# Kernel optimization log

Measured on AMD Instinct MI355X. Metric: run time of the kernel, lower is better.

## Reference

```python
import jax, jax.numpy as jnp
import numpy as np

N, E, R = 50000, 300000, 4
F_IN, H, G, T = 11, 256, 2048, 19
BN_EPS = 1e-5


def _init_lin(key, fan_in, fan_out, extra=()):
    k1, k2 = jax.random.split(key)
    s = 1.0 / np.sqrt(fan_in)
    W = jax.random.uniform(k1, extra + (fan_in, fan_out), jnp.float32, -s, s)
    b = jax.random.uniform(k2, extra + (fan_out,), jnp.float32, -s, s)
    return W, b


def setup_inputs() -> dict:
    key = jax.random.key(0)
    ks = jax.random.split(key, 32)
    inp = {
        "x": jax.random.normal(ks[0], (N, F_IN), jnp.float32),
        "edge_index": jax.random.randint(ks[1], (2, E), 0, N, jnp.int64),
        "edge_type": jax.random.randint(ks[2], (E,), 0, R, jnp.int64),
        "batch": jnp.sort(jax.random.randint(ks[3], (N,), 0, G, jnp.int64)),
    }
    ki = 4
    for li, fin in ((1, F_IN), (2, H), (3, H)):
        sw, sb = _init_lin(ks[ki], fin, H); ki += 1
        w1, b1 = _init_lin(ks[ki], fin, H, (R,)); ki += 1
        w2, b2 = _init_lin(ks[ki], H, H, (R,)); ki += 1
        inp[f"l{li}_sw"], inp[f"l{li}_sb"] = sw, sb
        inp[f"l{li}_w1"], inp[f"l{li}_b1"] = w1, b1
        inp[f"l{li}_g"] = jnp.ones((R, H), jnp.float32)
        inp[f"l{li}_bt"] = jnp.zeros((R, H), jnp.float32)
        inp[f"l{li}_w2"], inp[f"l{li}_b2"] = w2, b2
    inp["lin_w"], inp["lin_b"] = _init_lin(ks[ki], H, T)
    return inp


def _rgin_layer(x, src, dst, rel_mask, sw, sb, w1, b1, g, bt, w2, b2):
    # self-loop linear
    out = x @ sw + sb
    msg = x[src]  # [E, d] gather of source features
    for i in range(R):
        # per-relation masked scatter-add aggregation at target nodes
        agg = jax.ops.segment_sum(msg * rel_mask[:, i:i + 1], dst, num_segments=N)
        h = x + agg  # GIN with eps=0: (1+eps)*x + sum_neighbors
        h = h @ w1[i] + b1[i]
        # BatchNorm1d (training-mode batch stats, biased var)
        mu = jnp.mean(h, axis=0)
        var = jnp.var(h, axis=0)
        h = (h - mu) * jax.lax.rsqrt(var + BN_EPS) * g[i] + bt[i]
        h = jax.nn.relu(h)
        out = out + h @ w2[i] + b2[i]
    return out


def reference(x, edge_index, edge_type, batch,
              l1_sw, l1_sb, l1_w1, l1_b1, l1_g, l1_bt, l1_w2, l1_b2,
              l2_sw, l2_sb, l2_w1, l2_b1, l2_g, l2_bt, l2_w2, l2_b2,
              l3_sw, l3_sb, l3_w1, l3_b1, l3_g, l3_bt, l3_w2, l3_b2,
              lin_w, lin_b):
    src, dst = edge_index[0], edge_index[1]
    rel_mask = jax.nn.one_hot(edge_type, R, dtype=x.dtype)  # [E, R]
    h = jax.nn.relu(_rgin_layer(x, src, dst, rel_mask, l1_sw, l1_sb, l1_w1, l1_b1, l1_g, l1_bt, l1_w2, l1_b2))
    h = jax.nn.relu(_rgin_layer(h, src, dst, rel_mask, l2_sw, l2_sb, l2_w1, l2_b1, l2_g, l2_bt, l2_w2, l2_b2))
    h = jax.nn.relu(_rgin_layer(h, src, dst, rel_mask, l3_sw, l3_sb, l3_w1, l3_b1, l3_g, l3_bt, l3_w2, l3_b2))
    # global mean pool over graphs
    pooled = jax.ops.segment_sum(h, batch, num_segments=G)
    counts = jax.ops.segment_sum(jnp.ones((N,), h.dtype), batch, num_segments=G)
    pooled = pooled / jnp.maximum(counts, 1.0)[:, None]
    return pooled @ lin_w + lin_b
```

## Files before the change

### kernel.cpp

```cpp
#include <hip/hip_runtime.h>

static const int kN = 50000;
static const int kE = 300000;
static const int kG = 2048;
static const int kT = 19;
static const int kSeg = kN * 4;
static const int kScanB = (kSeg + 256) / 256;

typedef __bf16 bf16;
typedef __bf16 bf16x8 __attribute__((ext_vector_type(8)));
typedef __bf16 bf16x4 __attribute__((ext_vector_type(4)));
typedef float  f32x4  __attribute__((ext_vector_type(4)));

__global__ __launch_bounds__(512) void k_rgin1(
    const bf16* __restrict__ Pb, const int* __restrict__ srcidx,
    const int* __restrict__ row_ptr, const bf16* __restrict__ w1t,
    bf16* __restrict__ h1, float* __restrict__ stats)
{
    __shared__ bf16 As[64][264];
    const int t = threadIdx.x;
    const int r = blockIdx.y;
    const int m0 = blockIdx.x * 64;
    const int wave = t >> 6, lane = t & 63;
    const int l15 = lane & 15, lq = lane >> 4, koff = lq * 8;
    const int wn = wave * 32;

    const bf16* Bt = w1t + (long)r * 65536;
    const bf16* Bp[2];
#pragma unroll
    for (int j = 0; j < 2; ++j)
        Bp[j] = Bt + (long)(wn + j * 16 + l15) * 256 + koff;
    bf16x8 b0[2], b1[2];
#pragma unroll
    for (int j = 0; j < 2; ++j) b0[j] = *(const bf16x8*)(Bp[j]);

    {
        const int rbase = m0 + wave * 8;
        int i0s[8], i1s[8];
#pragma unroll
        for (int rr = 0; rr < 8; ++rr) {
            int dc = rbase + rr; if (dc >= kN) dc = kN - 1;
            int seg = dc * 4 + r;
            i0s[rr] = row_ptr[seg];
            i1s[rr] = row_ptr[seg + 1];
        }
#pragma unroll
        for (int rr = 0; rr < 8; ++rr) {
            int dc = rbase + rr; if (dc >= kN) dc = kN - 1;
            bf16x4 sv = ((const bf16x4*)(Pb + (long)dc * 256))[lane];
            f32x4 a = {(float)sv[0], (float)sv[1], (float)sv[2], (float)sv[3]};
            int i = i0s[rr], i1 = i1s[rr];
            for (; i + 1 < i1; i += 2) {
                int s0 = srcidx[i], s1 = srcidx[i + 1];
                bf16x4 v0 = ((const bf16x4*)(Pb + (long)s0 * 256))[lane];
                bf16x4 v1 = ((const bf16x4*)(Pb + (long)s1 * 256))[lane];
                a[0] += (float)v0[0] + (float)v1[0];
                a[1] += (float)v0[1] + (float)v1[1];
                a[2] += (float)v0[2] + (float)v1[2];
                a[3] += (float)v0[3] + (float)v1[3];
            }
            if (i < i1) {
                bf16x4 v0 = ((const bf16x4*)(Pb + (long)srcidx[i] * 256))[lane];
                a[0] += (float)v0[0]; a[1] += (float)v0[1];
                a[2] += (float)v0[2]; a[3] += (float)v0[3];
            }
            bf16x4 o = {(bf16)a[0], (bf16)a[1], (bf16)a[2], (bf16)a[3]};
            *(bf16x4*)&As[wave * 8 + rr][lane * 4] = o;
        }
    }
    __syncthreads();

    const bf16* Ar[4];
#pragma unroll
    for (int i = 0; i < 4; ++i) Ar[i] = &As[i * 16 + l15][koff];

    f32x4 acc[4][2];
#pragma unroll
    for (int i = 0; i < 4; ++i)
#pragma unroll
        for (int j = 0; j < 2; ++j) acc[i][j] = (f32x4){0.f, 0.f, 0.f, 0.f};

#pragma unroll
    for (int kt = 0; kt < 256; kt += 32) {
        int kn = kt + 32; if (kn >= 256) kn = 0;
#pragma unroll
        for (int j = 0; j < 2; ++j) b1[j] = *(const bf16x8*)(Bp[j] + kn);
        bf16x8 a[4];
#pragma unroll
        for (int i = 0; i < 4; ++i) a[i] = *(const bf16x8*)(Ar[i] + kt);
#pragma unroll
        for (int i = 0; i < 4; ++i)
#pragma unroll
            for (int j = 0; j < 2; ++j)
                acc[i][j] = __builtin_amdgcn_mfma_f32_16x16x32_bf16(a[i], b0[j], acc[i][j], 0, 0, 0);
#pragma unroll
        for (int j = 0; j < 2; ++j) b0[j] = b1[j];
    }

    const int cB = r * 256;
    float sv[2] = {0, 0}, qv[2] = {0, 0};
#pragma unroll
    for (int i = 0; i < 4; ++i) {
        int rowb = m0 + i * 16 + lq * 4;
#pragma unroll
        for (int rr = 0; rr < 4; ++rr) {
            int gm = rowb + rr;
            if (gm < kN) {
#pragma unroll
                for (int j = 0; j < 2; ++j) {
                    int gn = wn + j * 16 + l15;
                    bf16 bv = (bf16)acc[i][j][rr];
                    h1[(long)gm * 1024 + cB + gn] = bv;
                    float f = (float)bv;
                    sv[j] += f; qv[j] += f * f;
                }
            }
        }
    }
#pragma unroll
    for (int j = 0; j < 2; ++j) {
        float s = sv[j], q = qv[j];
        s += __shfl_xor(s, 16); s += __shfl_xor(s, 32);
        q += __shfl_xor(q, 16); q += __shfl_xor(q, 32);
        if (lq == 0) {
            int gn = cB + wn + j * 16 + l15;
            atomicAdd(&stats[gn], s);
            atomicAdd(&stats[1024 + gn], q);
        }
    }
}

__global__ __launch_bounds__(512) void k_l1gemm(
    const bf16* __restrict__ a1b, const bf16* __restrict__ w1tL1,
    bf16* __restrict__ h1, float* __restrict__ stats)
{
    const int t = threadIdx.x;
    const int r = blockIdx.y;
    const int m0 = blockIdx.x * 128;
    const int wave = t >> 6, lane = t & 63;
    const int l15 = lane & 15, lq = lane >> 4, koff = lq * 8;
    const int wm = (wave & 1) * 64, wn = (wave >> 1) * 64;

    bf16x8 a[4], b[4];
#pragma unroll
    for (int i = 0; i < 4; ++i) {
        int gm = m0 + wm + i * 16 + l15;
        if (gm >= kN) gm = kN - 1;
        a[i] = *(const bf16x8*)(a1b + ((long)r * kN + gm) * 32 + koff);
    }
#pragma unroll
    for (int j = 0; j < 4; ++j)
        b[j] = *(const bf16x8*)(w1tL1 + (long)r * 8192 + (long)(wn + j * 16 + l15) * 32 + koff);

    f32x4 acc[4][4];
#pragma unroll
    for (int i = 0; i < 4; ++i)
#pragma unroll
        for (int j = 0; j < 4; ++j)
            acc[i][j] = __builtin_amdgcn_mfma_f32_16x16x32_bf16(a[i], b[j],
                        (f32x4){0.f, 0.f, 0.f, 0.f}, 0, 0, 0);

    const int cB = r * 256;
    float sv[4] = {0,0,0,0}, qv[4] = {0,0,0,0};
#pragma unroll
    for (int i = 0; i < 4; ++i) {
        int rowb = m0 + wm + i * 16 + lq * 4;
#pragma unroll
        for (int rr = 0; rr < 4; ++rr) {
            int gm = rowb + rr;
            if (gm < kN) {
#pragma unroll
                for (int j = 0; j < 4; ++j) {
                    int gn = wn + j * 16 + l15;
                    bf16 bv = (bf16)acc[i][j][rr];
                    h1[(long)gm * 1024 + cB + gn] = bv;
                    float f = (float)bv;
                    sv[j] += f; qv[j] += f * f;
                }
            }
        }
    }
#pragma unroll
    for (int j = 0; j < 4; ++j) {
        float s = sv[j], q = qv[j];
        s += __shfl_xor(s, 16); s += __shfl_xor(s, 32);
        q += __shfl_xor(q, 16); q += __shfl_xor(q, 32);
        if (lq == 0) {
            int gn = cB + wn + j * 16 + l15;
            atomicAdd(&stats[gn], s);
            atomicAdd(&stats[1024 + gn], q);
        }
    }
}

template<int CHUNKS, int C1, bool PoolOut>
__global__ __launch_bounds__(256) void k_gemm2(
    const bf16* __restrict__ A1, int lda1,
    const bf16* __restrict__ A2,
    const bf16* __restrict__ Bt,
    bf16* __restrict__ Cout,
    int M, const float* __restrict__ bias,
    const float* __restrict__ scl, const float* __restrict__ shf,
    const int* __restrict__ batch, float* __restrict__ pooled)
{
    constexpr int K  = CHUNKS * 128;
    constexpr int KS = CHUNKS * 4;
    __shared__ bf16 As[2][64][136];
    const int t = threadIdx.x;
    const int wave = t >> 6, lane = t & 63;
    const int l15 = lane & 15, lq = lane >> 4, koff = lq * 8;
    const int wn = wave * 64;
    const int m0 = blockIdx.x * 64;

    const int srow = t >> 4;
    const int kg   = (t & 15) * 8;

    const bf16* Bp[4];
#pragma unroll
    for (int j = 0; j < 4; ++j)
        Bp[j] = Bt + (long)(wave * 4 + j) * KS * 512 + lane * 8;

    f32x4 acc[4][4];
#pragma unroll
    for (int i = 0; i < 4; ++i)
#pragma unroll
        for (int j = 0; j < 4; ++j) acc[i][j] = (f32x4){0.f, 0.f, 0.f, 0.f};

    auto ld_raw = [&](int c, bf16x8* rv, float4* sf) {
#pragma unroll
        for (int i = 0; i < 4; ++i) {
            int gm = m0 + srow + i * 16; if (gm >= M) gm = M - 1;
            if (c < C1) rv[i] = *(const bf16x8*)(A1 + (long)gm * lda1 + c * 128 + kg);
            else        rv[i] = *(const bf16x8*)(A2 + (long)gm * 1024 + (c - C1) * 128 + kg);
        }
        if (c >= C1) {
            int k2 = (c - C1) * 128 + kg;
            sf[0] = *(const float4*)(scl + k2);
            sf[1] = *(const float4*)(scl + k2 + 4);
            sf[2] = *(const float4*)(shf + k2);
            sf[3] = *(const float4*)(shf + k2 + 4);
        }
    };
    auto st_lds = [&](int c, const bf16x8* rv, const float4* sf, int sel) {
        float sa[8], ta[8];
        if (c >= C1) {
            sa[0]=sf[0].x; sa[1]=sf[0].y; sa[2]=sf[0].z; sa[3]=sf[0].w;
            sa[4]=sf[1].x; sa[5]=sf[1].y; sa[6]=sf[1].z; sa[7]=sf[1].w;
            ta[0]=sf[2].x; ta[1]=sf[2].y; ta[2]=sf[2].z; ta[3]=sf[2].w;
            ta[4]=sf[3].x; ta[5]=sf[3].y; ta[6]=sf[3].z; ta[7]=sf[3].w;
        }
#pragma unroll
        for (int i = 0; i < 4; ++i) {
            bf16x8 v = rv[i];
            if (c >= C1) {
                bf16x8 o;
#pragma unroll
                for (int u = 0; u < 8; ++u)
                    o[u] = (bf16)fmaxf(0.f, fmaf((float)v[u], sa[u], ta[u]));
                v = o;
            }
            *(bf16x8*)&As[sel][srow + i * 16][kg] = v;
        }
    };

    bf16x8 rv[4]; float4 sf[4];
    ld_raw(0, rv, sf);
    bf16x8 breg[2][4];
#pragma unroll
    for (int j = 0; j < 4; ++j) breg[0][j] = *(const bf16x8*)(Bp[j]);
#pragma unroll
    for (int j = 0; j < 4; ++j) breg[1][j] = *(const bf16x8*)(Bp[j] + 512);
    st_lds(0, rv, sf, 0);
    __syncthreads();

    for (int c = 0; c < CHUNKS; ++c) {
        const int sel = c & 1;
        if (c + 1 < CHUNKS) ld_raw(c + 1, rv, sf);
#pragma unroll
        for (int ks = 0; ks < 4; ++ks) {
            bf16x8 a[4], bu[4];
#pragma unroll
            for (int i = 0; i < 4; ++i)
                a[i] = *(const bf16x8*)&As[sel][i * 16 + l15][ks * 32 + koff];
#pragma unroll
            for (int j = 0; j < 4; ++j) bu[j] = breg[ks & 1][j];
            int knext = c * 4 + ks + 2; if (knext >= KS) knext = 0;
#pragma unroll
            for (int j = 0; j < 4; ++j)
                breg[ks & 1][j] = *(const bf16x8*)(Bp[j] + (long)knext * 512);
#pragma unroll
            for (int i = 0; i < 4; ++i)
#pragma unroll
                for (int j = 0; j < 4; ++j)
                    acc[i][j] = __builtin_amdgcn_mfma_f32_16x16x32_bf16(a[i], bu[j], acc[i][j], 0, 0, 0);
        }
        if (c + 1 < CHUNKS) {
            st_lds(c + 1, rv, sf, sel ^ 1);
            __syncthreads();
        }
    }

#pragma unroll
    for (int i = 0; i < 4; ++i) {
        int rowb = m0 + i * 16 + lq * 4;
#pragma unroll
        for (int rr = 0; rr < 4; ++rr) {
            int gm = rowb + rr;
            if (gm < M) {
                int g = PoolOut ? batch[gm] : 0;
#pragma unroll
                for (int j = 0; j < 4; ++j) {
                    int gn = wn + j * 16 + l15;
                    float v = fmaxf(acc[i][j][rr] + bias[gn], 0.f);
                    if (PoolOut) atomicAdd(&pooled[(long)g * 256 + gn], v);
                    else         Cout[(long)gm * 256 + gn] = (bf16)v;
                }
            }
        }
    }
}

__global__ void k_hist(const int* __restrict__ ei, const int* __restrict__ et,
                       int* __restrict__ hist)
{
    int e = blockIdx.x * 256 + threadIdx.x;
    if (e >= kE) return;
    atomicAdd(&hist[ei[kE + e] * 4 + et[e]], 1);
}

__global__ void k_scan1(const int* __restrict__ hist, int* __restrict__ bsum)
{
    __shared__ int sd[256];
    int i = blockIdx.x * 256 + threadIdx.x;
    sd[threadIdx.x] = (i < kSeg) ? hist[i] : 0;
    __syncthreads();
    for (int o = 128; o > 0; o >>= 1) {
        if (threadIdx.x < o) sd[threadIdx.x] += sd[threadIdx.x + o];
        __syncthreads();
    }
    if (threadIdx.x == 0) bsum[blockIdx.x] = sd[0];
}

__global__ __launch_bounds__(1024) void k_scan2(const int* __restrict__ bsum,
                                                int* __restrict__ boff)
{
    __shared__ int sd[1024];
    int t = threadIdx.x;
    sd[t] = (t < kScanB) ? bsum[t] : 0;
    __syncthreads();
    for (int o = 1; o < 1024; o <<= 1) {
        int v = (t >= o) ? sd[t - o] : 0;
        __syncthreads();
        sd[t] += v;
        __syncthreads();
    }
    if (t < kScanB) boff[t] = (t == 0) ? 0 : sd[t - 1];
}

__global__ void k_scan3(const int* __restrict__ hist, const int* __restrict__ boff,
                        int* __restrict__ row_ptr, int* __restrict__ cursor)
{
    __shared__ int sd[256];
    int i = blockIdx.x * 256 + threadIdx.x;
    int v = (i < kSeg) ? hist[i] : 0;
    sd[threadIdx.x] = v;
    __syncthreads();
    for (int o = 1; o < 256; o <<= 1) {
        int u = (threadIdx.x >= o) ? sd[threadIdx.x - o] : 0;
        __syncthreads();
        sd[threadIdx.x] += u;
        __syncthreads();
    }
    if (i <= kSeg) {
        int excl = boff[blockIdx.x] + sd[threadIdx.x] - v;
        row_ptr[i] = excl;
        if (i < kSeg) cursor[i] = excl;
    }
}

__global__ void k_fill(const int* __restrict__ ei, const int* __restrict__ et,
                       int* __restrict__ cursor, int* __restrict__ srcidx)
{
    int e = blockIdx.x * 256 + threadIdx.x;
    if (e >= kE) return;
    int key = ei[kE + e] * 4 + et[e];
    int pos = atomicAdd(&cursor[key], 1);
    srcidx[pos] = ei[e];
}

__global__ void k_agg11(const float* __restrict__ x, const int* __restrict__ srcidx,
                        const int* __restrict__ row_ptr, bf16* __restrict__ a1b)
{
    long gid = (long)blockIdx.x * 256 + threadIdx.x;
    if (gid >= (long)kSeg * 32) return;
    int ch  = (int)(gid & 31);
    int seg = (int)(gid >> 5);
    int d = seg >> 2, r = seg & 3;
    float acc = 0.f;
    if (ch < 11) {
        acc = x[(long)d * 11 + ch];
        int i0 = row_ptr[seg], i1 = row_ptr[seg + 1];
        for (int i = i0; i < i1; ++i) acc += x[(long)srcidx[i] * 11 + ch];
    }
    a1b[((long)r * kN + d) * 32 + ch] = (bf16)acc;
}

__global__ void k_xpad(const float* __restrict__ x, bf16* __restrict__ xb1)
{
    long gid = (long)blockIdx.x * 256 + threadIdx.x;
    if (gid >= (long)kN * 128) return;
    int c = (int)(gid & 127); long d = gid >> 7;
    xb1[gid] = (c < 11) ? (bf16)x[d * 11 + c] : (bf16)0.f;
}

__global__ void k_wt_s(const float* __restrict__ in, bf16* __restrict__ out,
                       int K, int N, int ldout, int coff)
{
    int i = blockIdx.x * 256 + threadIdx.x;
    if (i >= K * N) return;
    int n = i / K, k = i - n * K;
    out[(long)n * ldout + coff + k] = (bf16)in[(long)k * N + n];
}

__global__ void k_wt_f(const float* __restrict__ in, bf16* __restrict__ out,
                       int Kin, int k0, int KS)
{
    int i = blockIdx.x * 256 + threadIdx.x;
    if (i >= Kin * 256) return;
    int n = i & 255, krel = i >> 8;
    int k = k0 + krel;
    int blk = ((n >> 6) * 4 + ((n >> 4) & 3)) * KS + (k >> 5);
    int idx = blk * 512 + ((k >> 3) & 3) * 128 + (n & 15) * 8 + (k & 7);
    out[idx] = (bf16)in[(long)krel * 256 + n];
}

__global__ void k_wtL1(const float* __restrict__ w1, bf16* __restrict__ out)
{
    int i = blockIdx.x * 256 + threadIdx.x;
    if (i >= 4 * 256 * 32) return;
    int r = i >> 13, rem = i & 8191, n = rem >> 5, k = rem & 31;
    out[i] = (k < 11) ? (bf16)w1[(long)r * 11 * 256 + (long)k * 256 + n] : (bf16)0.f;
}

__global__ void k_bn_params(const float* __restrict__ stats,
                            const float* __restrict__ g, const float* __restrict__ bt,
                            float* __restrict__ scl, float* __restrict__ shf)
{
    int c = blockIdx.x * 256 + threadIdx.x;
    const float invN = 1.0f / (float)kN;
    float mu  = stats[c] * invN;
    float var = stats[1024 + c] * invN - mu * mu;
    float sc  = g[c] * rsqrtf(var + 1e-5f);
    scl[c] = sc;
    shf[c] = bt[c] - mu * sc;
}

__global__ void k_bias_total(const float* sb0, const float* b20,
                             const float* sb1, const float* b21,
                             const float* sb2, const float* b22,
                             float* __restrict__ btt)
{
    int l = blockIdx.x, j = threadIdx.x;
    const float* sb = (l == 0) ? sb0 : (l == 1) ? sb1 : sb2;
    const float* b2 = (l == 0) ? b20 : (l == 1) ? b21 : b22;
    float v = sb[j];
#pragma unroll
    for (int r = 0; r < 4; ++r) v += b2[r * 256 + j];
    btt[l * 256 + j] = v;
}

__global__ void k_counts(const int* __restrict__ batch, float* __restrict__ counts)
{
    int v = blockIdx.x * 256 + threadIdx.x;
    if (v < kN) atomicAdd(&counts[batch[v]], 1.0f);
}

__global__ __launch_bounds__(64) void k_head(const float* __restrict__ pooled,
                                             const float* __restrict__ counts,
                                             const float* __restrict__ lw,
                                             const float* __restrict__ lb,
                                             float* __restrict__ out)
{
    int g = blockIdx.x;
    int l = threadIdx.x;
    float inv = 1.0f / fmaxf(counts[g], 1.0f);
    float acc[kT];
#pragma unroll
    for (int t = 0; t < kT; ++t) acc[t] = 0.f;
    for (int k = l; k < 256; k += 64) {
        float p = pooled[((long)g << 8) + k] * inv;
#pragma unroll
        for (int t = 0; t < kT; ++t) acc[t] = fmaf(p, lw[k * kT + t], acc[t]);
    }
#pragma unroll
    for (int off = 32; off > 0; off >>= 1)
#pragma unroll
        for (int t = 0; t < kT; ++t) acc[t] += __shfl_down(acc[t], off);
    if (l == 0) {
#pragma unroll
        for (int t = 0; t < kT; ++t) out[(long)g * kT + t] = acc[t] + lb[t];
    }
}

extern "C" void kernel_launch(void* const* d_in, const int* in_sizes, int n_in,
                              void* d_out, int out_size, void* d_ws, size_t ws_size,
                              hipStream_t stream)
{
    const float* x     = (const float*)d_in[0];
    const int*   ei    = (const int*)d_in[1];
    const int*   et    = (const int*)d_in[2];
    const int*   batch = (const int*)d_in[3];

    const float *sw[3], *sb[3], *w1[3], *gmm[3], *btm[3], *w2[3], *b2[3];
    for (int l = 0; l < 3; ++l) {
        int b = 4 + l * 8;
        sw[l]  = (const float*)d_in[b + 0];
        sb[l]  = (const float*)d_in[b + 1];
        w1[l]  = (const float*)d_in[b + 2];
        gmm[l] = (const float*)d_in[b + 4];
        btm[l] = (const float*)d_in[b + 5];
        w2[l]  = (const float*)d_in[b + 6];
        b2[l]  = (const float*)d_in[b + 7];
    }
    const float* lin_w = (const float*)d_in[28];
    const float* lin_b = (const float*)d_in[29];
    float* out = (float*)d_out;
    (void)in_sizes; (void)n_in; (void)out_size;

    char* wsb = (char*)d_ws;
    size_t off = 0;
    auto alloc = [&](size_t bytes) { void* p = wsb + off; off = (off + bytes + 255) & ~(size_t)255; return p; };
    bf16*  Pb0    = (bf16*) alloc((size_t)kN * 256 * 2);
    bf16*  Pb1    = (bf16*) alloc((size_t)kN * 256 * 2);
    bf16*  h1     = (bf16*) alloc((size_t)kN * 1024 * 2);
    bf16*  a1b    = (bf16*) alloc((size_t)4 * kN * 32 * 2);
    bf16*  xb1    = (bf16*) alloc((size_t)kN * 128 * 2);
    bf16*  w1t    = (bf16*) alloc((size_t)2 * 4 * 65536 * 2);
    bf16*  w1tL1  = (bf16*) alloc((size_t)4 * 256 * 32 * 2);
    bf16*  Bc0    = (bf16*) alloc((size_t)256 * 1152 * 2);
    bf16*  Bc1    = (bf16*) alloc((size_t)256 * 1280 * 2);
    bf16*  Bc2    = (bf16*) alloc((size_t)256 * 1280 * 2);
    int*   hist   = (int*)  alloc((size_t)(kSeg + 1) * 4);
    int*   row_ptr= (int*)  alloc((size_t)(kSeg + 1) * 4);
    int*   cursor = (int*)  alloc((size_t)kSeg * 4);
    int*   srcidx = (int*)  alloc((size_t)kE * 4);
    int*   bsum   = (int*)  alloc((size_t)kScanB * 4);
    int*   boff   = (int*)  alloc((size_t)kScanB * 4);
    float* stats  = (float*)alloc(2048 * 4);
    float* scl    = (float*)alloc(1024 * 4);
    float* shf    = (float*)alloc(1024 * 4);
    float* btt    = (float*)alloc(3 * 256 * 4);
    float* pooled = (float*)alloc((size_t)kG * 256 * 4);
    float* counts = (float*)alloc(kG * 4);
    if (ws_size < off) return;

    const dim3 gL1((kN + 127) / 128, 4);
    const dim3 gR((kN + 63) / 64, 4);
    const dim3 g2((kN + 63) / 64);

    hipMemsetAsync(hist, 0, (size_t)(kSeg + 1) * 4, stream);
    k_hist<<<(kE + 255) / 256, 256, 0, stream>>>(ei, et, hist);
    k_scan1<<<kScanB, 256, 0, stream>>>(hist, bsum);
    k_scan2<<<1, 1024, 0, stream>>>(bsum, boff);
    k_scan3<<<kScanB, 256, 0, stream>>>(hist, boff, row_ptr, cursor);
    k_fill<<<(kE + 255) / 256, 256, 0, stream>>>(ei, et, cursor, srcidx);

    k_bias_total<<<3, 256, 0, stream>>>(sb[0], b2[0], sb[1], b2[1], sb[2], b2[2], btt);
    k_xpad<<<(int)(((long)kN * 128 + 255) / 256), 256, 0, stream>>>(x, xb1);
    k_wtL1<<<(4 * 256 * 32 + 255) / 256, 256, 0, stream>>>(w1[0], w1tL1);
    for (int l = 1; l < 3; ++l)
        for (int r = 0; r < 4; ++r)
            k_wt_s<<<256, 256, 0, stream>>>(w1[l] + (long)r * 65536,
                                            w1t + (long)(l - 1) * 4 * 65536 + (long)r * 65536,
                                            256, 256, 256, 0);
    hipMemsetAsync(Bc0, 0, (size_t)256 * 1152 * 2, stream);
    k_wt_f<<<(11 * 256 + 255) / 256, 256, 0, stream>>>(sw[0], Bc0, 11, 0, 36);
    k_wt_f<<<1024, 256, 0, stream>>>(w2[0], Bc0, 1024, 128, 36);
    k_wt_f<<<256, 256, 0, stream>>>(sw[1], Bc1, 256, 0, 40);
    k_wt_f<<<1024, 256, 0, stream>>>(w2[1], Bc1, 1024, 256, 40);
    k_wt_f<<<256, 256, 0, stream>>>(sw[2], Bc2, 256, 0, 40);
    k_wt_f<<<1024, 256, 0, stream>>>(w2[2], Bc2, 1024, 256, 40);

    k_counts<<<(kN + 255) / 256, 256, 0, stream>>>(batch, counts);
    hipMemsetAsync(pooled, 0, (size_t)kG * 256 * 4, stream);

    k_agg11<<<(int)(((long)kSeg * 32 + 255) / 256), 256, 0, stream>>>(x, srcidx, row_ptr, a1b);
    hipMemsetAsync(stats, 0, 2048 * 4, stream);
    k_l1gemm<<<gL1, 512, 0, stream>>>(a1b, w1tL1, h1, stats);
    k_bn_params<<<4, 256, 0, stream>>>(stats, gmm[0], btm[0], scl, shf);
    k_gemm2<9, 1, false><<<g2, 256, 0, stream>>>(xb1, 128, h1, Bc0,
                                                 Pb0, kN, btt + 0, scl, shf, nullptr, nullptr);

    hipMemsetAsync(stats, 0, 2048 * 4, stream);
    k_rgin1<<<gR, 512, 0, stream>>>(Pb0, srcidx, row_ptr, w1t, h1, stats);
    k_bn_params<<<4, 256, 0, stream>>>(stats, gmm[1], btm[1], scl, shf);
    k_gemm2<10, 2, false><<<g2, 256, 0, stream>>>(Pb0, 256, h1, Bc1,
                                                  Pb1, kN, btt + 256, scl, shf, nullptr, nullptr);

    hipMemsetAsync(stats, 0, 2048 * 4, stream);
    k_rgin1<<<gR, 512, 0, stream>>>(Pb1, srcidx, row_ptr, w1t + (size_t)4 * 65536, h1, stats);
    k_bn_params<<<4, 256, 0, stream>>>(stats, gmm[2], btm[2], scl, shf);
    k_gemm2<10, 2, true><<<g2, 256, 0, stream>>>(Pb1, 256, h1, Bc2,
                                                 nullptr, kN, btt + 512, scl, shf, batch, pooled);

    k_head<<<kG, 64, 0, stream>>>(pooled, counts, lin_w, lin_b, out);
}
```

Measured before the change: 913.2 us.

## Hand-schedule gemm2 main loop with explicit waitcnts, setprio, and LDS-cached BN params

Rewrites the k_gemm2 K-loop as unrolled phases. Each phase reads A from LDS, waits only on specific vmcnt levels for the prefetched B registers, and issues the MFMAs under raised priority, with sched_barriers fixing the order. The BN scale/shift vectors are staged once into LDS instead of reloaded from global per chunk, and the last chunk is peeled so it issues no wasted prefetch. The aim is tighter overlap of global loads with MFMA work, at the cost of fragile hand-counted vmcnt values and extra LDS use.

Measured after the change: 888.1 us, median of 3. -2.8%, faster.

```diff
diff --git a/kernel.cpp b/kernel.cpp
--- a/kernel.cpp
+++ b/kernel.cpp
@@ -193,6 +193,24 @@
     }
 }
 
+#define KS_PHASE(SEL, KSI, BREG, VM) do {                                     \
+    bf16x8 a_[4];                                                             \
+    _Pragma("unroll")                                                         \
+    for (int i_ = 0; i_ < 4; ++i_)                                            \
+        a_[i_] = *(const bf16x8*)&As[SEL][i_ * 16 + l15][(KSI) * 32 + koff];  \
+    asm volatile("s_waitcnt vmcnt(" #VM ")" ::: "memory");                    \
+    __builtin_amdgcn_sched_barrier(0);                                        \
+    __builtin_amdgcn_s_setprio(1);                                            \
+    _Pragma("unroll")                                                         \
+    for (int i_ = 0; i_ < 4; ++i_)                                            \
+        _Pragma("unroll")                                                     \
+        for (int j_ = 0; j_ < 4; ++j_)                                        \
+            acc[i_][j_] = __builtin_amdgcn_mfma_f32_16x16x32_bf16(            \
+                a_[i_], BREG[j_], acc[i_][j_], 0, 0, 0);                      \
+    __builtin_amdgcn_s_setprio(0);                                            \
+    __builtin_amdgcn_sched_barrier(0);                                        \
+} while (0)
+
 template<int CHUNKS, int C1, bool PoolOut>
 __global__ __launch_bounds__(256) void k_gemm2(
     const bf16* __restrict__ A1, int lda1,
@@ -203,9 +221,10 @@
     const float* __restrict__ scl, const float* __restrict__ shf,
     const int* __restrict__ batch, float* __restrict__ pooled)
 {
-    constexpr int K  = CHUNKS * 128;
     constexpr int KS = CHUNKS * 4;
     __shared__ bf16 As[2][64][136];
+    __shared__ float sclL[1024];
+    __shared__ float shfL[1024];
     const int t = threadIdx.x;
     const int wave = t >> 6, lane = t & 63;
     const int l15 = lane & 15, lq = lane >> 4, koff = lq * 8;
@@ -226,78 +245,101 @@
 #pragma unroll
         for (int j = 0; j < 4; ++j) acc[i][j] = (f32x4){0.f, 0.f, 0.f, 0.f};
 
-    auto ld_raw = [&](int c, bf16x8* rv, float4* sf) {
+    bf16x8 rv[4];
+    auto ld_A = [&](int c) {
 #pragma unroll
         for (int i = 0; i < 4; ++i) {
             int gm = m0 + srow + i * 16; if (gm >= M) gm = M - 1;
-            if (c < C1) rv[i] = *(const bf16x8*)(A1 + (long)gm * lda1 + c * 128 + kg);
-            else        rv[i] = *(const bf16x8*)(A2 + (long)gm * 1024 + (c - C1) * 128 + kg);
-        }
+            const bf16* p = (c < C1)
+                ? (A1 + (long)gm * lda1 + c * 128 + kg)
+                : (A2 + (long)gm * 1024 + (c - C1) * 128 + kg);
+            rv[i] = *(const bf16x8*)p;
+        }
+    };
+    auto st_lds = [&](int c, int sel) {
         if (c >= C1) {
             int k2 = (c - C1) * 128 + kg;
-            sf[0] = *(const float4*)(scl + k2);
-            sf[1] = *(const float4*)(scl + k2 + 4);
-            sf[2] = *(const float4*)(shf + k2);
-            sf[3] = *(const float4*)(shf + k2 + 4);
-        }
-    };
-    auto st_lds = [&](int c, const bf16x8* rv, const float4* sf, int sel) {
-        float sa[8], ta[8];
-        if (c >= C1) {
-            sa[0]=sf[0].x; sa[1]=sf[0].y; sa[2]=sf[0].z; sa[3]=sf[0].w;
-            sa[4]=sf[1].x; sa[5]=sf[1].y; sa[6]=sf[1].z; sa[7]=sf[1].w;
-            ta[0]=sf[2].x; ta[1]=sf[2].y; ta[2]=sf[2].z; ta[3]=sf[2].w;
-            ta[4]=sf[3].x; ta[5]=sf[3].y; ta[6]=sf[3].z; ta[7]=sf[3].w;
-        }
-#pragma unroll
-        for (int i = 0; i < 4; ++i) {
-            bf16x8 v = rv[i];
-            if (c >= C1) {
-                bf16x8 o;
+            float4 s0 = *(const float4*)&sclL[k2];
+            float4 s1 = *(const float4*)&sclL[k2 + 4];
+            float4 t0 = *(const float4*)&shfL[k2];
+            float4 t1 = *(const float4*)&shfL[k2 + 4];
+            float sa[8] = {s0.x, s0.y, s0.z, s0.w, s1.x, s1.y, s1.z, s1.w};
+            float ta[8] = {t0.x, t0.y, t0.z, t0.w, t1.x, t1.y, t1.z, t1.w};
+#pragma unroll
+            for (int i = 0; i < 4; ++i) {
+                bf16x8 v = rv[i]; bf16x8 o;
 #pragma unroll
                 for (int u = 0; u < 8; ++u)
                     o[u] = (bf16)fmaxf(0.f, fmaf((float)v[u], sa[u], ta[u]));
-                v = o;
+                *(bf16x8*)&As[sel][srow + i * 16][kg] = o;
             }
-            *(bf16x8*)&As[sel][srow + i * 16][kg] = v;
+        } else {
+#pragma unroll
+            for (int i = 0; i < 4; ++i)
+                *(bf16x8*)&As[sel][srow + i * 16][kg] = rv[i];
         }
     };
 
-    bf16x8 rv[4]; float4 sf[4];
-    ld_raw(0, rv, sf);
-    bf16x8 breg[2][4];
-#pragma unroll
-    for (int j = 0; j < 4; ++j) breg[0][j] = *(const bf16x8*)(Bp[j]);
-#pragma unroll
-    for (int j = 0; j < 4; ++j) breg[1][j] = *(const bf16x8*)(Bp[j] + 512);
-    st_lds(0, rv, sf, 0);
-    __syncthreads();
-
-    for (int c = 0; c < CHUNKS; ++c) {
+    bf16x8 breg0[4], breg1[4];
+
+    {
+        const float* src = (t < 128) ? (scl + t * 8) : (shf + (t - 128) * 8);
+        float*       dst = (t < 128) ? (sclL + t * 8) : (shfL + (t - 128) * 8);
+        float4 f0 = *(const float4*)src;
+        float4 f1 = *(const float4*)(src + 4);
+        ld_A(0);
+#pragma unroll
+        for (int j = 0; j < 4; ++j) breg0[j] = *(const bf16x8*)(Bp[j]);
+#pragma unroll
+        for (int j = 0; j < 4; ++j) breg1[j] = *(const bf16x8*)(Bp[j] + 512);
+        asm volatile("s_waitcnt vmcnt(12)" ::: "memory");
+        __builtin_amdgcn_sched_barrier(0);
+        *(float4*)dst = f0; *(float4*)(dst + 4) = f1;
+        asm volatile("s_waitcnt vmcnt(8)" ::: "memory");
+        __builtin_amdgcn_sched_barrier(0);
+        st_lds(0, 0);
+        asm volatile("s_waitcnt lgkmcnt(0)" ::: "memory");
+        __builtin_amdgcn_s_barrier();
+    }
+
+    for (int c = 0; c < CHUNKS - 1; ++c) {
         const int sel = c & 1;
-        if (c + 1 < CHUNKS) ld_raw(c + 1, rv, sf);
-#pragma unroll
-        for (int ks = 0; ks < 4; ++ks) {
-            bf16x8 a[4], bu[4];
-#pragma unroll
-            for (int i = 0; i < 4; ++i)
-                a[i] = *(const bf16x8*)&As[sel][i * 16 + l15][ks * 32 + koff];
-#pragma unroll
-            for (int j = 0; j < 4; ++j) bu[j] = breg[ks & 1][j];
-            int knext = c * 4 + ks + 2; if (knext >= KS) knext = 0;
-#pragma unroll
-            for (int j = 0; j < 4; ++j)
-                breg[ks & 1][j] = *(const bf16x8*)(Bp[j] + (long)knext * 512);
-#pragma unroll
-            for (int i = 0; i < 4; ++i)
-#pragma unroll
-                for (int j = 0; j < 4; ++j)
-                    acc[i][j] = __builtin_amdgcn_mfma_f32_16x16x32_bf16(a[i], bu[j], acc[i][j], 0, 0, 0);
-        }
-        if (c + 1 < CHUNKS) {
-            st_lds(c + 1, rv, sf, sel ^ 1);
-            __syncthreads();
-        }
+        KS_PHASE(sel, 0, breg0, 4);
+#pragma unroll
+        for (int j = 0; j < 4; ++j)
+            breg0[j] = *(const bf16x8*)(Bp[j] + (long)(4 * c + 2) * 512);
+        ld_A(c + 1);
+        KS_PHASE(sel, 1, breg1, 8);
+#pragma unroll
+        for (int j = 0; j < 4; ++j)
+            breg1[j] = *(const bf16x8*)(Bp[j] + (long)(4 * c + 3) * 512);
+        KS_PHASE(sel, 2, breg0, 8);
+#pragma unroll
+        for (int j = 0; j < 4; ++j)
+            breg0[j] = *(const bf16x8*)(Bp[j] + (long)(4 * c + 4) * 512);
+        KS_PHASE(sel, 3, breg1, 4);
+#pragma unroll
+        for (int j = 0; j < 4; ++j)
+            breg1[j] = *(const bf16x8*)(Bp[j] + (long)(4 * c + 5) * 512);
+        asm volatile("s_waitcnt vmcnt(8)" ::: "memory");
+        __builtin_amdgcn_sched_barrier(0);
+        st_lds(c + 1, sel ^ 1);
+        asm volatile("s_waitcnt lgkmcnt(0)" ::: "memory");
+        __builtin_amdgcn_s_barrier();
+    }
+
+    {
+        const int c = CHUNKS - 1, sel = c & 1;
+        KS_PHASE(sel, 0, breg0, 4);
+#pragma unroll
+        for (int j = 0; j < 4; ++j)
+            breg0[j] = *(const bf16x8*)(Bp[j] + (long)(4 * c + 2) * 512);
+        KS_PHASE(sel, 1, breg1, 4);
+#pragma unroll
+        for (int j = 0; j < 4; ++j)
+            breg1[j] = *(const bf16x8*)(Bp[j] + (long)(4 * c + 3) * 512);
+        KS_PHASE(sel, 2, breg0, 4);
+        KS_PHASE(sel, 3, breg1, 0);
     }
 
 #pragma unroll
```

## Halve gemm2 row tile and stage K in two halves with swizzled LDS

Applied to the files above, without the earlier changes.

The second-stage GEMM drops from 64-row to 32-row blocks, doubling the grid. Instead of double-buffered 128-wide K chunks with a barrier per chunk, it loads half of the K range into LDS, syncs, computes, then loads the second half. LDS addressing uses an XOR swizzle to avoid bank conflicts. This cuts barriers and accumulator registers so more blocks can be resident, but each block reuses the B operand over fewer rows and global loads no longer overlap with the MFMA work.

Measured after the change: 1.105 ms. 21.0% more time.

```diff
diff --git a/kernel.cpp b/kernel.cpp
--- a/kernel.cpp
+++ b/kernel.cpp
@@ -203,105 +203,106 @@
     const float* __restrict__ scl, const float* __restrict__ shf,
     const int* __restrict__ batch, float* __restrict__ pooled)
 {
-    constexpr int K  = CHUNKS * 128;
-    constexpr int KS = CHUNKS * 4;
-    __shared__ bf16 As[2][64][136];
+    constexpr int KS   = CHUNKS * 4;
+    constexpr int HC0  = (CHUNKS + 1) / 2;
+    constexpr int ROWB = HC0 * 256;
+    __shared__ bf16 As[32 * HC0 * 128];
+
     const int t = threadIdx.x;
     const int wave = t >> 6, lane = t & 63;
     const int l15 = lane & 15, lq = lane >> 4, koff = lq * 8;
     const int wn = wave * 64;
-    const int m0 = blockIdx.x * 64;
-
+    const int m0 = blockIdx.x * 32;
     const int srow = t >> 4;
     const int kg   = (t & 15) * 8;
 
+    auto lds_off = [&](int row, int colrel) {
+        return row * ROWB + ((colrel * 2) ^ ((row & 7) << 4));
+    };
+
     const bf16* Bp[4];
 #pragma unroll
     for (int j = 0; j < 4; ++j)
         Bp[j] = Bt + (long)(wave * 4 + j) * KS * 512 + lane * 8;
 
-    f32x4 acc[4][4];
-#pragma unroll
-    for (int i = 0; i < 4; ++i)
+    f32x4 acc[2][4];
+#pragma unroll
+    for (int i = 0; i < 2; ++i)
 #pragma unroll
         for (int j = 0; j < 4; ++j) acc[i][j] = (f32x4){0.f, 0.f, 0.f, 0.f};
 
-    auto ld_raw = [&](int c, bf16x8* rv, float4* sf) {
-#pragma unroll
-        for (int i = 0; i < 4; ++i) {
-            int gm = m0 + srow + i * 16; if (gm >= M) gm = M - 1;
-            if (c < C1) rv[i] = *(const bf16x8*)(A1 + (long)gm * lda1 + c * 128 + kg);
-            else        rv[i] = *(const bf16x8*)(A2 + (long)gm * 1024 + (c - C1) * 128 + kg);
-        }
-        if (c >= C1) {
-            int k2 = (c - C1) * 128 + kg;
-            sf[0] = *(const float4*)(scl + k2);
-            sf[1] = *(const float4*)(scl + k2 + 4);
-            sf[2] = *(const float4*)(shf + k2);
-            sf[3] = *(const float4*)(shf + k2 + 4);
-        }
-    };
-    auto st_lds = [&](int c, const bf16x8* rv, const float4* sf, int sel) {
-        float sa[8], ta[8];
-        if (c >= C1) {
-            sa[0]=sf[0].x; sa[1]=sf[0].y; sa[2]=sf[0].z; sa[3]=sf[0].w;
-            sa[4]=sf[1].x; sa[5]=sf[1].y; sa[6]=sf[1].z; sa[7]=sf[1].w;
-            ta[0]=sf[2].x; ta[1]=sf[2].y; ta[2]=sf[2].z; ta[3]=sf[2].w;
-            ta[4]=sf[3].x; ta[5]=sf[3].y; ta[6]=sf[3].z; ta[7]=sf[3].w;
-        }
-#pragma unroll
-        for (int i = 0; i < 4; ++i) {
-            bf16x8 v = rv[i];
-            if (c >= C1) {
-                bf16x8 o;
-#pragma unroll
-                for (int u = 0; u < 8; ++u)
-                    o[u] = (bf16)fmaxf(0.f, fmaf((float)v[u], sa[u], ta[u]));
-                v = o;
+    bf16x8 breg0[4], breg1[4];
+#pragma unroll
+    for (int j = 0; j < 4; ++j) breg0[j] = *(const bf16x8*)(Bp[j]);
+#pragma unroll
+    for (int j = 0; j < 4; ++j) breg1[j] = *(const bf16x8*)(Bp[j] + 512);
+
+#define KSTEP(GKS_, BREG_) do {                                               \
+    const int colrel_ = ((GKS_) - c0 * 4) * 32 + koff;                        \
+    bf16x8 a0_ = *(const bf16x8*)((const char*)As + lds_off(l15, colrel_));   \
+    bf16x8 a1_ = *(const bf16x8*)((const char*)As + lds_off(16 + l15, colrel_)); \
+    bf16x8 bu_[4];                                                            \
+    _Pragma("unroll")                                                         \
+    for (int j_ = 0; j_ < 4; ++j_) bu_[j_] = BREG_[j_];                       \
+    int nk_ = (GKS_) + 2; if (nk_ >= KS) nk_ = 0;                             \
+    _Pragma("unroll")                                                         \
+    for (int j_ = 0; j_ < 4; ++j_)                                            \
+        BREG_[j_] = *(const bf16x8*)(Bp[j_] + (long)nk_ * 512);               \
+    _Pragma("unroll")                                                         \
+    for (int j_ = 0; j_ < 4; ++j_) {                                          \
+        acc[0][j_] = __builtin_amdgcn_mfma_f32_16x16x32_bf16(a0_, bu_[j_], acc[0][j_], 0, 0, 0); \
+        acc[1][j_] = __builtin_amdgcn_mfma_f32_16x16x32_bf16(a1_, bu_[j_], acc[1][j_], 0, 0, 0); \
+    }                                                                         \
+} while (0)
+
+#pragma unroll
+    for (int h = 0; h < 2; ++h) {
+        const int c0 = h ? HC0 : 0;
+        const int cN = h ? CHUNKS : HC0;
+#pragma unroll
+        for (int cc = 0; cc < cN - c0; ++cc) {
+            const int c = c0 + cc;
+            const int col = c * 128 + kg;
+            if (c < C1) {
+#pragma unroll
+                for (int p = 0; p < 2; ++p) {
+                    int gm = m0 + srow + p * 16; if (gm >= M) gm = M - 1;
+                    bf16x8 v = *(const bf16x8*)(A1 + (long)gm * lda1 + col);
+                    *(bf16x8*)((char*)As + lds_off(srow + p * 16, cc * 128 + kg)) = v;
+                }
+            } else {
+                const int k2 = col - C1 * 128;
+                float4 s0 = *(const float4*)(scl + k2);
+                float4 s1 = *(const float4*)(scl + k2 + 4);
+                float4 t0 = *(const float4*)(shf + k2);
+                float4 t1 = *(const float4*)(shf + k2 + 4);
+                float sa[8] = {s0.x,s0.y,s0.z,s0.w,s1.x,s1.y,s1.z,s1.w};
+                float ta[8] = {t0.x,t0.y,t0.z,t0.w,t1.x,t1.y,t1.z,t1.w};
+#pragma unroll
+                for (int p = 0; p < 2; ++p) {
+                    int gm = m0 + srow + p * 16; if (gm >= M) gm = M - 1;
+                    bf16x8 v = *(const bf16x8*)(A2 + (long)gm * 1024 + k2);
+                    bf16x8 o;
+#pragma unroll
+                    for (int u = 0; u < 8; ++u)
+                        o[u] = (bf16)fmaxf(0.f, fmaf((float)v[u], sa[u], ta[u]));
+                    *(bf16x8*)((char*)As + lds_off(srow + p * 16, cc * 128 + kg)) = o;
+                }
             }
-            *(bf16x8*)&As[sel][srow + i * 16][kg] = v;
-        }
-    };
-
-    bf16x8 rv[4]; float4 sf[4];
-    ld_raw(0, rv, sf);
-    bf16x8 breg[2][4];
-#pragma unroll
-    for (int j = 0; j < 4; ++j) breg[0][j] = *(const bf16x8*)(Bp[j]);
-#pragma unroll
-    for (int j = 0; j < 4; ++j) breg[1][j] = *(const bf16x8*)(Bp[j] + 512);
-    st_lds(0, rv, sf, 0);
-    __syncthreads();
-
-    for (int c = 0; c < CHUNKS; ++c) {
-        const int sel = c & 1;
-        if (c + 1 < CHUNKS) ld_raw(c + 1, rv, sf);
-#pragma unroll
-        for (int ks = 0; ks < 4; ++ks) {
-            bf16x8 a[4], bu[4];
-#pragma unroll
-            for (int i = 0; i < 4; ++i)
-                a[i] = *(const bf16x8*)&As[sel][i * 16 + l15][ks * 32 + koff];
-#pragma unroll
-            for (int j = 0; j < 4; ++j) bu[j] = breg[ks & 1][j];
-            int knext = c * 4 + ks + 2; if (knext >= KS) knext = 0;
-#pragma unroll
-            for (int j = 0; j < 4; ++j)
-                breg[ks & 1][j] = *(const bf16x8*)(Bp[j] + (long)knext * 512);
-#pragma unroll
-            for (int i = 0; i < 4; ++i)
-#pragma unroll
-                for (int j = 0; j < 4; ++j)
-                    acc[i][j] = __builtin_amdgcn_mfma_f32_16x16x32_bf16(a[i], bu[j], acc[i][j], 0, 0, 0);
-        }
-        if (c + 1 < CHUNKS) {
-            st_lds(c + 1, rv, sf, sel ^ 1);
-            __syncthreads();
-        }
-    }
-
-#pragma unroll
-    for (int i = 0; i < 4; ++i) {
+        }
+        __syncthreads();
+        const int nks = (cN - c0) * 4;
+#pragma unroll
+        for (int s = 0; s < nks; s += 2) {
+            KSTEP(c0 * 4 + s,     breg0);
+            KSTEP(c0 * 4 + s + 1, breg1);
+        }
+        if (h == 0) __syncthreads();
+    }
+#undef KSTEP
+
+#pragma unroll
+    for (int i = 0; i < 2; ++i) {
         int rowb = m0 + i * 16 + lq * 4;
 #pragma unroll
         for (int rr = 0; rr < 4; ++rr) {
@@ -556,7 +557,7 @@
 
     const dim3 gL1((kN + 127) / 128, 4);
     const dim3 gR((kN + 63) / 64, 4);
-    const dim3 g2((kN + 63) / 64);
+    const dim3 g2((kN + 31) / 32);
 
     hipMemsetAsync(hist, 0, (size_t)(kSeg + 1) * 4, stream);
     k_hist<<<(kE + 255) / 256, 256, 0, stream>>>(ei, et, hist);
```

## Store h1 in MFMA fragment layout, fold BN scale into W2, drop LDS staging

Applied to the files above, without the earlier changes.

The first GEMM outputs and the padded input are now written in a pre-tiled MFMA A-fragment layout, so the second GEMM loads fragments straight from global memory without LDS staging or barriers. The BatchNorm scale is folded into the W2 weights, which are rebuilt after each stats pass, so the activation transform reduces to an add followed by ReLU. The intent is to remove shared-memory traffic, synchronisation and per-element FMA work from the main GEMM. In exchange it adds scattered 2-byte stores in the producers and extra weight-repack launches. The identity bt/sc - mu breaks down if the scale is zero or negative, and the fixed-size fragment buffer relies on the padded panel count.

New measurement: 1.121 ms. +22.8%, slower.

```diff
diff --git a/kernel.cpp b/kernel.cpp
--- a/kernel.cpp
+++ b/kernel.cpp
@@ -12,10 +12,15 @@
 typedef __bf16 bf16x4 __attribute__((ext_vector_type(4)));
 typedef float  f32x4  __attribute__((ext_vector_type(4)));
 
+__device__ __forceinline__ long fragA_idx(int row, int k, int KSR) {
+    return ((long)(row >> 4) * KSR + (k >> 5)) * 512
+         + ((k >> 3) & 3) * 128 + (row & 15) * 8 + (k & 7);
+}
+
 __global__ __launch_bounds__(512) void k_rgin1(
     const bf16* __restrict__ Pb, const int* __restrict__ srcidx,
     const int* __restrict__ row_ptr, const bf16* __restrict__ w1t,
-    bf16* __restrict__ h1, float* __restrict__ stats)
+    bf16* __restrict__ h1F, float* __restrict__ stats)
 {
     __shared__ bf16 As[64][264];
     const int t = threadIdx.x;
@@ -110,7 +115,8 @@
                 for (int j = 0; j < 2; ++j) {
                     int gn = wn + j * 16 + l15;
                     bf16 bv = (bf16)acc[i][j][rr];
-                    h1[(long)gm * 1024 + cB + gn] = bv;
+                    int kk = cB + gn;
+                    h1F[fragA_idx(gm, kk, 32)] = bv;
                     float f = (float)bv;
                     sv[j] += f; qv[j] += f * f;
                 }
@@ -132,7 +138,7 @@
 
 __global__ __launch_bounds__(512) void k_l1gemm(
     const bf16* __restrict__ a1b, const bf16* __restrict__ w1tL1,
-    bf16* __restrict__ h1, float* __restrict__ stats)
+    bf16* __restrict__ h1F, float* __restrict__ stats)
 {
     const int t = threadIdx.x;
     const int r = blockIdx.y;
@@ -173,7 +179,8 @@
                 for (int j = 0; j < 4; ++j) {
                     int gn = wn + j * 16 + l15;
                     bf16 bv = (bf16)acc[i][j][rr];
-                    h1[(long)gm * 1024 + cB + gn] = bv;
+                    int kk = cB + gn;
+                    h1F[fragA_idx(gm, kk, 32)] = bv;
                     float f = (float)bv;
                     sv[j] += f; qv[j] += f * f;
                 }
@@ -193,32 +200,32 @@
     }
 }
 
-template<int CHUNKS, int C1, bool PoolOut>
-__global__ __launch_bounds__(256) void k_gemm2(
-    const bf16* __restrict__ A1, int lda1,
-    const bf16* __restrict__ A2,
+template<int CHUNKS, int C1, bool A1F, bool PoolOut>
+__global__ __launch_bounds__(256, 3) void k_gemm2(
+    const bf16* __restrict__ A1,
+    const bf16* __restrict__ A2F,
     const bf16* __restrict__ Bt,
     bf16* __restrict__ Cout,
     int M, const float* __restrict__ bias,
-    const float* __restrict__ scl, const float* __restrict__ shf,
+    const float* __restrict__ u,
     const int* __restrict__ batch, float* __restrict__ pooled)
 {
-    constexpr int K  = CHUNKS * 128;
-    constexpr int KS = CHUNKS * 4;
-    __shared__ bf16 As[2][64][136];
+    constexpr int KS  = CHUNKS * 4;
+    constexpr int KS1 = C1 * 4;
+    constexpr int KS2 = KS - KS1;
+    static_assert(KS2 == 32, "h1F packed with KSR=32");
+
     const int t = threadIdx.x;
     const int wave = t >> 6, lane = t & 63;
     const int l15 = lane & 15, lq = lane >> 4, koff = lq * 8;
-    const int wn = wave * 64;
+    const int cg = wave;
     const int m0 = blockIdx.x * 64;
-
-    const int srow = t >> 4;
-    const int kg   = (t & 15) * 8;
+    const int mp = m0 >> 4;
 
     const bf16* Bp[4];
 #pragma unroll
     for (int j = 0; j < 4; ++j)
-        Bp[j] = Bt + (long)(wave * 4 + j) * KS * 512 + lane * 8;
+        Bp[j] = Bt + ((long)(cg * 4 + j) * KS) * 512 + lane * 8;
 
     f32x4 acc[4][4];
 #pragma unroll
@@ -226,78 +233,49 @@
 #pragma unroll
         for (int j = 0; j < 4; ++j) acc[i][j] = (f32x4){0.f, 0.f, 0.f, 0.f};
 
-    auto ld_raw = [&](int c, bf16x8* rv, float4* sf) {
+#pragma unroll
+    for (int ks = 0; ks < KS1; ++ks) {
+        bf16x8 a[4], b[4];
 #pragma unroll
         for (int i = 0; i < 4; ++i) {
-            int gm = m0 + srow + i * 16; if (gm >= M) gm = M - 1;
-            if (c < C1) rv[i] = *(const bf16x8*)(A1 + (long)gm * lda1 + c * 128 + kg);
-            else        rv[i] = *(const bf16x8*)(A2 + (long)gm * 1024 + (c - C1) * 128 + kg);
-        }
-        if (c >= C1) {
-            int k2 = (c - C1) * 128 + kg;
-            sf[0] = *(const float4*)(scl + k2);
-            sf[1] = *(const float4*)(scl + k2 + 4);
-            sf[2] = *(const float4*)(shf + k2);
-            sf[3] = *(const float4*)(shf + k2 + 4);
-        }
-    };
-    auto st_lds = [&](int c, const bf16x8* rv, const float4* sf, int sel) {
-        float sa[8], ta[8];
-        if (c >= C1) {
-            sa[0]=sf[0].x; sa[1]=sf[0].y; sa[2]=sf[0].z; sa[3]=sf[0].w;
-            sa[4]=sf[1].x; sa[5]=sf[1].y; sa[6]=sf[1].z; sa[7]=sf[1].w;
-            ta[0]=sf[2].x; ta[1]=sf[2].y; ta[2]=sf[2].z; ta[3]=sf[2].w;
-            ta[4]=sf[3].x; ta[5]=sf[3].y; ta[6]=sf[3].z; ta[7]=sf[3].w;
-        }
+            if (A1F) {
+                a[i] = *(const bf16x8*)(A1 + ((long)(mp + i) * KS1 + ks) * 512 + lane * 8);
+            } else {
+                int gm = m0 + i * 16 + l15; if (gm >= M) gm = M - 1;
+                a[i] = *(const bf16x8*)(A1 + (long)gm * 256 + ks * 32 + koff);
+            }
+        }
+#pragma unroll
+        for (int j = 0; j < 4; ++j) b[j] = *(const bf16x8*)(Bp[j] + (long)ks * 512);
+#pragma unroll
+        for (int i = 0; i < 4; ++i)
+#pragma unroll
+            for (int j = 0; j < 4; ++j)
+                acc[i][j] = __builtin_amdgcn_mfma_f32_16x16x32_bf16(a[i], b[j], acc[i][j], 0, 0, 0);
+    }
+
+#pragma unroll 4
+    for (int k2 = 0; k2 < KS2; ++k2) {
+        float4 u0 = *(const float4*)(u + k2 * 32 + koff);
+        float4 u1 = *(const float4*)(u + k2 * 32 + koff + 4);
+        float u8[8] = {u0.x, u0.y, u0.z, u0.w, u1.x, u1.y, u1.z, u1.w};
+        bf16x8 a[4], b[4];
 #pragma unroll
         for (int i = 0; i < 4; ++i) {
-            bf16x8 v = rv[i];
-            if (c >= C1) {
-                bf16x8 o;
-#pragma unroll
-                for (int u = 0; u < 8; ++u)
-                    o[u] = (bf16)fmaxf(0.f, fmaf((float)v[u], sa[u], ta[u]));
-                v = o;
-            }
-            *(bf16x8*)&As[sel][srow + i * 16][kg] = v;
-        }
-    };
-
-    bf16x8 rv[4]; float4 sf[4];
-    ld_raw(0, rv, sf);
-    bf16x8 breg[2][4];
-#pragma unroll
-    for (int j = 0; j < 4; ++j) breg[0][j] = *(const bf16x8*)(Bp[j]);
-#pragma unroll
-    for (int j = 0; j < 4; ++j) breg[1][j] = *(const bf16x8*)(Bp[j] + 512);
-    st_lds(0, rv, sf, 0);
-    __syncthreads();
-
-    for (int c = 0; c < CHUNKS; ++c) {
-        const int sel = c & 1;
-        if (c + 1 < CHUNKS) ld_raw(c + 1, rv, sf);
-#pragma unroll
-        for (int ks = 0; ks < 4; ++ks) {
-            bf16x8 a[4], bu[4];
-#pragma unroll
-            for (int i = 0; i < 4; ++i)
-                a[i] = *(const bf16x8*)&As[sel][i * 16 + l15][ks * 32 + koff];
-#pragma unroll
-            for (int j = 0; j < 4; ++j) bu[j] = breg[ks & 1][j];
-            int knext = c * 4 + ks + 2; if (knext >= KS) knext = 0;
+            bf16x8 h = *(const bf16x8*)(A2F + ((long)(mp + i) * 32 + k2) * 512 + lane * 8);
+            bf16x8 o;
+#pragma unroll
+            for (int e = 0; e < 8; ++e)
+                o[e] = (bf16)fmaxf((float)h[e] + u8[e], 0.f);
+            a[i] = o;
+        }
+#pragma unroll
+        for (int j = 0; j < 4; ++j) b[j] = *(const bf16x8*)(Bp[j] + (long)(KS1 + k2) * 512);
+#pragma unroll
+        for (int i = 0; i < 4; ++i)
 #pragma unroll
             for (int j = 0; j < 4; ++j)
-                breg[ks & 1][j] = *(const bf16x8*)(Bp[j] + (long)knext * 512);
-#pragma unroll
-            for (int i = 0; i < 4; ++i)
-#pragma unroll
-                for (int j = 0; j < 4; ++j)
-                    acc[i][j] = __builtin_amdgcn_mfma_f32_16x16x32_bf16(a[i], bu[j], acc[i][j], 0, 0, 0);
-        }
-        if (c + 1 < CHUNKS) {
-            st_lds(c + 1, rv, sf, sel ^ 1);
-            __syncthreads();
-        }
+                acc[i][j] = __builtin_amdgcn_mfma_f32_16x16x32_bf16(a[i], b[j], acc[i][j], 0, 0, 0);
     }
 
 #pragma unroll
@@ -310,7 +288,7 @@
                 int g = PoolOut ? batch[gm] : 0;
 #pragma unroll
                 for (int j = 0; j < 4; ++j) {
-                    int gn = wn + j * 16 + l15;
+                    int gn = cg * 64 + j * 16 + l15;
                     float v = fmaxf(acc[i][j][rr] + bias[gn], 0.f);
                     if (PoolOut) atomicAdd(&pooled[(long)g * 256 + gn], v);
                     else         Cout[(long)gm * 256 + gn] = (bf16)v;
@@ -405,12 +383,14 @@
     a1b[((long)r * kN + d) * 32 + ch] = (bf16)acc;
 }
 
-__global__ void k_xpad(const float* __restrict__ x, bf16* __restrict__ xb1)
+__global__ void k_xpad(const float* __restrict__ x, bf16* __restrict__ xb1F)
 {
     long gid = (long)blockIdx.x * 256 + threadIdx.x;
     if (gid >= (long)kN * 128) return;
-    int c = (int)(gid & 127); long d = gid >> 7;
-    xb1[gid] = (c < 11) ? (bf16)x[d * 11 + c] : (bf16)0.f;
+    int c = (int)(gid & 127); int d = (int)(gid >> 7);
+    long idx = ((long)(d >> 4) * 4 + (c >> 5)) * 512
+             + ((c >> 3) & 3) * 128 + (d & 15) * 8 + (c & 7);
+    xb1F[idx] = (c < 11) ? (bf16)x[(long)d * 11 + c] : (bf16)0.f;
 }
 
 __global__ void k_wt_s(const float* __restrict__ in, bf16* __restrict__ out,
@@ -434,6 +414,18 @@
     out[idx] = (bf16)in[(long)krel * 256 + n];
 }
 
+__global__ void k_wt_fs(const float* __restrict__ in, const float* __restrict__ s,
+                        bf16* __restrict__ out, int Kin, int k0, int KS)
+{
+    int i = blockIdx.x * 256 + threadIdx.x;
+    if (i >= Kin * 256) return;
+    int n = i & 255, krel = i >> 8;
+    int k = k0 + krel;
+    int blk = ((n >> 6) * 4 + ((n >> 4) & 3)) * KS + (k >> 5);
+    int idx = blk * 512 + ((k >> 3) & 3) * 128 + (n & 15) * 8 + (k & 7);
+    out[idx] = (bf16)(in[(long)krel * 256 + n] * s[krel]);
+}
+
 __global__ void k_wtL1(const float* __restrict__ w1, bf16* __restrict__ out)
 {
     int i = blockIdx.x * 256 + threadIdx.x;
@@ -444,7 +436,7 @@
 
 __global__ void k_bn_params(const float* __restrict__ stats,
                             const float* __restrict__ g, const float* __restrict__ bt,
-                            float* __restrict__ scl, float* __restrict__ shf)
+                            float* __restrict__ scl, float* __restrict__ uu)
 {
     int c = blockIdx.x * 256 + threadIdx.x;
     const float invN = 1.0f / (float)kN;
@@ -452,7 +444,7 @@
     float var = stats[1024 + c] * invN - mu * mu;
     float sc  = g[c] * rsqrtf(var + 1e-5f);
     scl[c] = sc;
-    shf[c] = bt[c] - mu * sc;
+    uu[c]  = bt[c] / sc - mu;
 }
 
 __global__ void k_bias_total(const float* sb0, const float* b20,
@@ -527,14 +519,15 @@
     float* out = (float*)d_out;
     (void)in_sizes; (void)n_in; (void)out_size;
 
+    const int kPanels = 3128;
     char* wsb = (char*)d_ws;
     size_t off = 0;
     auto alloc = [&](size_t bytes) { void* p = wsb + off; off = (off + bytes + 255) & ~(size_t)255; return p; };
     bf16*  Pb0    = (bf16*) alloc((size_t)kN * 256 * 2);
     bf16*  Pb1    = (bf16*) alloc((size_t)kN * 256 * 2);
-    bf16*  h1     = (bf16*) alloc((size_t)kN * 1024 * 2);
+    bf16*  h1F    = (bf16*) alloc((size_t)kPanels * 32 * 512 * 2);
     bf16*  a1b    = (bf16*) alloc((size_t)4 * kN * 32 * 2);
-    bf16*  xb1    = (bf16*) alloc((size_t)kN * 128 * 2);
+    bf16*  xb1F   = (bf16*) alloc((size_t)kPanels * 4 * 512 * 2);
     bf16*  w1t    = (bf16*) alloc((size_t)2 * 4 * 65536 * 2);
     bf16*  w1tL1  = (bf16*) alloc((size_t)4 * 256 * 32 * 2);
     bf16*  Bc0    = (bf16*) alloc((size_t)256 * 1152 * 2);
@@ -548,7 +541,7 @@
     int*   boff   = (int*)  alloc((size_t)kScanB * 4);
     float* stats  = (float*)alloc(2048 * 4);
     float* scl    = (float*)alloc(1024 * 4);
-    float* shf    = (float*)alloc(1024 * 4);
+    float* uu     = (float*)alloc(1024 * 4);
     float* btt    = (float*)alloc(3 * 256 * 4);
     float* pooled = (float*)alloc((size_t)kG * 256 * 4);
     float* counts = (float*)alloc(kG * 4);
@@ -566,7 +559,7 @@
     k_fill<<<(kE + 255) / 256, 256, 0, stream>>>(ei, et, cursor, srcidx);
 
     k_bias_total<<<3, 256, 0, stream>>>(sb[0], b2[0], sb[1], b2[1], sb[2], b2[2], btt);
-    k_xpad<<<(int)(((long)kN * 128 + 255) / 256), 256, 0, stream>>>(x, xb1);
+    k_xpad<<<(int)(((long)kN * 128 + 255) / 256), 256, 0, stream>>>(x, xb1F);
     k_wtL1<<<(4 * 256 * 32 + 255) / 256, 256, 0, stream>>>(w1[0], w1tL1);
     for (int l = 1; l < 3; ++l)
         for (int r = 0; r < 4; ++r)
@@ -575,33 +568,33 @@
                                             256, 256, 256, 0);
     hipMemsetAsync(Bc0, 0, (size_t)256 * 1152 * 2, stream);
     k_wt_f<<<(11 * 256 + 255) / 256, 256, 0, stream>>>(sw[0], Bc0, 11, 0, 36);
-    k_wt_f<<<1024, 256, 0, stream>>>(w2[0], Bc0, 1024, 128, 36);
     k_wt_f<<<256, 256, 0, stream>>>(sw[1], Bc1, 256, 0, 40);
-    k_wt_f<<<1024, 256, 0, stream>>>(w2[1], Bc1, 1024, 256, 40);
     k_wt_f<<<256, 256, 0, stream>>>(sw[2], Bc2, 256, 0, 40);
-    k_wt_f<<<1024, 256, 0, stream>>>(w2[2], Bc2, 1024, 256, 40);
 
     k_counts<<<(kN + 255) / 256, 256, 0, stream>>>(batch, counts);
     hipMemsetAsync(pooled, 0, (size_t)kG * 256 * 4, stream);
 
     k_agg11<<<(int)(((long)kSeg * 32 + 255) / 256), 256, 0, stream>>>(x, srcidx, row_ptr, a1b);
     hipMemsetAsync(stats, 0, 2048 * 4, stream);
-    k_l1gemm<<<gL1, 512, 0, stream>>>(a1b, w1tL1, h1, stats);
-    k_bn_params<<<4, 256, 0, stream>>>(stats, gmm[0], btm[0], scl, shf);
-    k_gemm2<9, 1, false><<<g2, 256, 0, stream>>>(xb1, 128, h1, Bc0,
-                                                 Pb0, kN, btt + 0, scl, shf, nullptr, nullptr);
+    k_l1gemm<<<gL1, 512, 0, stream>>>(a1b, w1tL1, h1F, stats);
+    k_bn_params<<<4, 256, 0, stream>>>(stats, gmm[0], btm[0], scl, uu);
+    k_wt_fs<<<1024, 256, 0, stream>>>(w2[0], scl, Bc0, 1024, 128, 36);
+    k_gemm2<9, 1, true, false><<<g2, 256, 0, stream>>>(xb1F, h1F, Bc0,
+                                                       Pb0, kN, btt + 0, uu, nullptr, nullptr);
 
     hipMemsetAsync(stats, 0, 2048 * 4, stream);
-    k_rgin1<<<gR, 512, 0, stream>>>(Pb0, srcidx, row_ptr, w1t, h1, stats);
-    k_bn_params<<<4, 256, 0, stream>>>(stats, gmm[1], btm[1], scl, shf);
-    k_gemm2<10, 2, false><<<g2, 256, 0, stream>>>(Pb0, 256, h1, Bc1,
-                                                  Pb1, kN, btt + 256, scl, shf, nullptr, nullptr);
+    k_rgin1<<<gR, 512, 0, stream>>>(Pb0, srcidx, row_ptr, w1t, h1F, stats);
+    k_bn_params<<<4, 256, 0, stream>>>(stats, gmm[1], btm[1], scl, uu);
+    k_wt_fs<<<1024, 256, 0, stream>>>(w2[1], scl, Bc1, 1024, 256, 40);
+    k_gemm2<10, 2, false, false><<<g2, 256, 0, stream>>>(Pb0, h1F, Bc1,
+                                                         Pb1, kN, btt + 256, uu, nullptr, nullptr);
 
     hipMemsetAsync(stats, 0, 2048 * 4, stream);
-    k_rgin1<<<gR, 512, 0, stream>>>(Pb1, srcidx, row_ptr, w1t + (size_t)4 * 65536, h1, stats);
-    k_bn_params<<<4, 256, 0, stream>>>(stats, gmm[2], btm[2], scl, shf);
-    k_gemm2<10, 2, true><<<g2, 256, 0, stream>>>(Pb1, 256, h1, Bc2,
-                                                 nullptr, kN, btt + 512, scl, shf, batch, pooled);
+    k_rgin1<<<gR, 512, 0, stream>>>(Pb1, srcidx, row_ptr, w1t + (size_t)4 * 65536, h1F, stats);
+    k_bn_params<<<4, 256, 0, stream>>>(stats, gmm[2], btm[2], scl, uu);
+    k_wt_fs<<<1024, 256, 0, stream>>>(w2[2], scl, Bc2, 1024, 256, 40);
+    k_gemm2<10, 2, false, true><<<g2, 256, 0, stream>>>(Pb1, h1F, Bc2,
+                                                        nullptr, kN, btt + 512, uu, batch, pooled);
 
     k_head<<<kG, 64, 0, stream>>>(pooled, counts, lin_w, lin_b, out);
 }
```
